# Kernel optimization log

Hardware: AMD Instinct MI355X
Metric: run time of the kernel (lower is better)

The kernel has to match this reference:

```python
import jax, jax.numpy as jnp
import numpy as np

ALPHA = 0.2  # LeakyReLU slope in GAT
OUT_SLOPE = 0.01  # default nn.LeakyyReLU slope for self.out
B, E, IN_DIM, HID, HEADS = 4, 2048, 32, 18, 3
DH = HID // HEADS  # per-head out dim = 6


def _leaky(x, slope):
    return jnp.where(x > 0, x, slope * x)


def _gat_head(x, adj, W, a):
    # x: [B,E,in], W: [in,dh], a: [2*dh,1]
    h = jnp.einsum('bei,id->bed', x, W)                      # [B,E,dh]
    d = h.shape[-1]
    # score[b,i,j] = leakyrelu(a . concat(h_i, h_j)) = leakyrelu(h_i.a1 + h_j.a2)
    e1 = jnp.einsum('bed,d->be', h, a[:d, 0])
    e2 = jnp.einsum('bed,d->be', h, a[d:, 0])
    score = _leaky(e1[:, :, None] + e2[:, None, :], ALPHA)   # [B,E,E]
    scores = jnp.where(adj == 1.0, score, 0.0)
    logits = jnp.where(adj > 0.0, scores, -30.0)
    att = jax.nn.softmax(logits, axis=2)                     # softmax over j
    # h_prime[b,j,d] = sum_i att[b,i,j] * h[b,i,d]  (torch sums over dim=1)
    h_prime = jnp.einsum('bij,bid->bjd', att, h)
    return jax.nn.elu(h_prime)  # concat=True -> elu


def _gat_multihead(x, adj, Ws, As):
    # Ws: [H,in,dh], As: [H,2*dh,1]
    outs = jax.vmap(lambda W, a: _gat_head(x, adj, W, a))(Ws, As)  # [H,B,E,dh]
    H, b, e, d = outs.shape
    return jnp.moveaxis(outs, 0, 2).reshape(b, e, H * d)  # concat heads last-dim


def _gcn(x, adj2d, W, b):
    return adj2d @ (x @ W) + b


def setup_inputs() -> dict:
    key = jax.random.key(0)
    ks = jax.random.split(key, 16)
    node_input = jax.random.normal(ks[0], (B, E, IN_DIM), jnp.float32)
    uv_filed = jax.random.normal(ks[1], (B, E, IN_DIM), jnp.float32)
    adj = jax.random.randint(ks[2], (B, E, E), 0, 2).astype(jnp.float32)
    s = 0.1
    Wt1 = jax.random.normal(ks[3], (HEADS, IN_DIM, DH), jnp.float32) * s
    at1 = jax.random.normal(ks[4], (HEADS, 2 * DH, 1), jnp.float32) * s
    Wt2 = jax.random.normal(ks[5], (HEADS, IN_DIM, DH), jnp.float32) * s
    at2 = jax.random.normal(ks[6], (HEADS, 2 * DH, 1), jnp.float32) * s
    Wg1 = jax.random.normal(ks[7], (HID, 16), jnp.float32) * s
    bg1 = jnp.zeros((16,), jnp.float32)
    Wg2 = jax.random.normal(ks[8], (16, 2), jnp.float32) * s
    bg2 = jnp.zeros((2,), jnp.float32)
    Wo1 = jax.random.normal(ks[9], (HID, 16), jnp.float32) * s
    bo1 = jnp.zeros((16,), jnp.float32)
    Wo2 = jax.random.normal(ks[10], (16, 2), jnp.float32) * s
    bo2 = jnp.zeros((2,), jnp.float32)
    return dict(node_input=node_input, uv_filed=uv_filed, adj=adj,
                Wt1=Wt1, at1=at1, Wt2=Wt2, at2=at2,
                Wg1=Wg1, bg1=bg1, Wg2=Wg2, bg2=bg2,
                Wo1=Wo1, bo1=bo1, Wo2=Wo2, bo2=bo2)


def reference(node_input, uv_filed, adj, Wt1, at1, Wt2, at2,
              Wg1, bg1, Wg2, bg2, Wo1, bo1, Wo2, bo2):
    h = _gat_multihead(node_input, adj, Wt1, at1)  # [B,E,18]
    o = _gat_multihead(uv_filed, adj, Wt2, at2)    # [B,E,18]
    a0 = adj[0]
    Y = jax.nn.relu(_gcn(h[0], a0, Wg1, bg1))
    O = jax.nn.relu(_gcn(o[0], a0, Wo1, bo1))
    Y = _gcn(Y, a0, Wg2, bg2)
    O = _gcn(O, a0, Wo2, bo2)
    return (jax.nn.log_softmax(Y, axis=1), _leaky(O, OUT_SLOPE))
```

## Files before the change

### kernel.cpp

```cpp
#include <hip/hip_runtime.h>
#include <hip/hip_bf16.h>


__global__ __launch_bounds__(256) void k0_bitmask(
    const float* __restrict__ adj0, unsigned int* __restrict__ bm) {
  int lane = threadIdx.x & 63, w = threadIdx.x >> 6;
  int row = blockIdx.x * 4 + w;
  const float* arow = adj0 + (size_t)row * 2048;
#pragma unroll 4
  for (int it = 0; it < 32; ++it) {
    float v = arow[it * 64 + lane];
    unsigned long long mask = __ballot(v == 1.0f);
    if (lane == 0) bm[row * 64 + it * 2] = (unsigned int)mask;
    else if (lane == 32) bm[row * 64 + it * 2 + 1] = (unsigned int)(mask >> 32);
  }
}

__global__ __launch_bounds__(256) void k1_features(
    const float* __restrict__ node, const float* __restrict__ uv,
    const float* __restrict__ Wt1, const float* __restrict__ at1,
    const float* __restrict__ Wt2, const float* __restrict__ at2,
    float* __restrict__ hcol, float* __restrict__ pack1, float* __restrict__ pack2) {
  __shared__ float sW[192];
  __shared__ float sA[12];
  int b = blockIdx.x;
  int g = b / 24;
  int h = (b / 8) % 3;
  int e = (b % 8) * 256 + threadIdx.x;
  const float* W = (g ? Wt2 : Wt1) + h * 192;
  const float* A = (g ? at2 : at1) + h * 12;
  const float* x = (g ? uv : node) + e * 32;
  if (threadIdx.x < 192) sW[threadIdx.x] = W[threadIdx.x];
  if (threadIdx.x < 12) sA[threadIdx.x] = A[threadIdx.x];
  __syncthreads();
  float xv[32];
#pragma unroll
  for (int i = 0; i < 32; ++i) xv[i] = x[i];
  float hv[6];
#pragma unroll
  for (int d = 0; d < 6; ++d) hv[d] = 0.f;
#pragma unroll
  for (int i = 0; i < 32; ++i)
#pragma unroll
    for (int d = 0; d < 6; ++d) hv[d] += xv[i] * sW[i * 6 + d];
  float e1 = 0.f, e2 = 0.f;
#pragma unroll
  for (int d = 0; d < 6; ++d) {
    e1 += hv[d] * sA[d];
    e2 += hv[d] * sA[6 + d];
  }
  int c = g * 3 + h;
#pragma unroll
  for (int d = 0; d < 6; ++d) hcol[(c * 6 + d) * 2048 + e] = hv[d];
  pack1[c * 2048 + e] = e1;
  pack1[(6 + c) * 2048 + e] = __expf(e1);
  pack1[(12 + c) * 2048 + e] = __expf(0.2f * e1);
  pack2[c * 2048 + e] = e2;
  pack2[(6 + c) * 2048 + e] = __expf(e2);
  pack2[(12 + c) * 2048 + e] = __expf(0.2f * e2);
}

__global__ __launch_bounds__(384) void k2_rowsum(
    const unsigned int* __restrict__ bm, const float* __restrict__ pack1,
    const float* __restrict__ pack2, float* __restrict__ invrs) {
  int tid = threadIdx.x;
  int c = tid >> 6, lane = tid & 63;
  int i0 = blockIdx.x * 8;
  const float4* p2_4 = (const float4*)pack2;
  float e1r[8], p1r[8], q1r[8], sum[8];
#pragma unroll
  for (int r = 0; r < 8; ++r) {
    e1r[r] = pack1[c * 2048 + i0 + r];
    p1r[r] = pack1[(6 + c) * 2048 + i0 + r];
    q1r[r] = pack1[(12 + c) * 2048 + i0 + r];
    sum[r] = 0.f;
  }
  int sh = (lane & 7) * 4;
#pragma unroll
  for (int it = 0; it < 8; ++it) {
    int j4 = it * 64 + lane;
    float4 e2 = p2_4[c * 512 + j4];
    float4 p2 = p2_4[(6 + c) * 512 + j4];
    float4 q2 = p2_4[(12 + c) * 512 + j4];
    int wbase = it * 8 + (lane >> 3);
    float abx, aby, abz, abw;
#pragma unroll
    for (int r = 0; r < 8; ++r) {
      unsigned int wd = bm[(i0 + r) * 64 + wbase] >> sh;
      { float e = e1r[r] + e2.x; bool p = e > 0.f;
        abx = (p ? p1r[r] : q1r[r]) * (p ? p2.x : q2.x); }
      { float e = e1r[r] + e2.y; bool p = e > 0.f;
        aby = (p ? p1r[r] : q1r[r]) * (p ? p2.y : q2.y); }
      { float e = e1r[r] + e2.z; bool p = e > 0.f;
        abz = (p ? p1r[r] : q1r[r]) * (p ? p2.z : q2.z); }
      { float e = e1r[r] + e2.w; bool p = e > 0.f;
        abw = (p ? p1r[r] : q1r[r]) * (p ? p2.w : q2.w); }
      float s = ((wd & 1u) ? abx : 0.f) + ((wd & 2u) ? aby : 0.f) +
                ((wd & 4u) ? abz : 0.f) + ((wd & 8u) ? abw : 0.f);
      sum[r] += s;
    }
  }
#pragma unroll
  for (int r = 0; r < 8; ++r) {
#pragma unroll
    for (int off = 32; off > 0; off >>= 1) sum[r] += __shfl_down(sum[r], off);
  }
  if (lane == 0) {
#pragma unroll
    for (int r = 0; r < 8; ++r) invrs[c * 2048 + i0 + r] = 1.0f / sum[r];
  }
}

__global__ __launch_bounds__(384) void k3_hprime(
    const unsigned int* __restrict__ bm, const float* __restrict__ hcol,
    const float* __restrict__ pack1, const float* __restrict__ pack2,
    const float* __restrict__ invrs, float* __restrict__ hp_part) {
  __shared__ float4 sPack[6 * 64];
  __shared__ float sHS[6 * 64 * 8];
  __shared__ unsigned int sM[64 * 4];
  float4* sHS4 = (float4*)sHS;
  int tid = threadIdx.x;
  int c6 = tid >> 6, jl = tid & 63;
  int j0 = blockIdx.x * 128;
  int jA = j0 + jl, jB = jA + 64;
  float e2A = pack2[c6 * 2048 + jA];
  float p2A = pack2[(6 + c6) * 2048 + jA];
  float q2A = pack2[(12 + c6) * 2048 + jA];
  float e2B = pack2[c6 * 2048 + jB];
  float p2B = pack2[(6 + c6) * 2048 + jB];
  float q2B = pack2[(12 + c6) * 2048 + jB];
  float aA0 = 0.f, aA1 = 0.f, aA2 = 0.f, aA3 = 0.f, aA4 = 0.f, aA5 = 0.f;
  float aB0 = 0.f, aB1 = 0.f, aB2 = 0.f, aB3 = 0.f, aB4 = 0.f, aB5 = 0.f;
  int hi = jl >> 5;
  int shj = jl & 31;
  int ibeg = blockIdx.y * 128;
  for (int i0 = ibeg; i0 < ibeg + 128; i0 += 64) {
    __syncthreads();
    {
      int cc = c6, ii = jl;
      float e1 = pack1[cc * 2048 + i0 + ii];
      float p1 = pack1[(6 + cc) * 2048 + i0 + ii];
      float q1 = pack1[(12 + cc) * 2048 + i0 + ii];
      sPack[cc * 64 + ii] = make_float4(e1, p1, q1, 0.f);
      float iv = invrs[cc * 2048 + i0 + ii];
#pragma unroll
      for (int d = 0; d < 6; ++d)
        sHS[(cc * 64 + ii) * 8 + d] = hcol[(cc * 6 + d) * 2048 + i0 + ii] * iv;
      sHS[(cc * 64 + ii) * 8 + 6] = 0.f;
      sHS[(cc * 64 + ii) * 8 + 7] = 0.f;
    }
    if (tid < 256) sM[tid] = bm[(size_t)(i0 + (tid >> 2)) * 64 + (j0 >> 5) + (tid & 3)];
    __syncthreads();
#pragma unroll 8
    for (int ii = 0; ii < 64; ++ii) {
      float4 pk = sPack[c6 * 64 + ii];
      float4 h0 = sHS4[(c6 * 64 + ii) * 2];
      float4 h1 = sHS4[(c6 * 64 + ii) * 2 + 1];
      unsigned int wdA = sM[ii * 4 + hi];
      unsigned int wdB = sM[ii * 4 + 2 + hi];
      {
        float e = pk.x + e2A; bool p = e > 0.f;
        float ab = (p ? pk.y : pk.z) * (p ? p2A : q2A);
        float wgt = ((wdA >> shj) & 1u) ? ab : 0.f;
        aA0 += wgt * h0.x; aA1 += wgt * h0.y; aA2 += wgt * h0.z;
        aA3 += wgt * h0.w; aA4 += wgt * h1.x; aA5 += wgt * h1.y;
      }
      {
        float e = pk.x + e2B; bool p = e > 0.f;
        float ab = (p ? pk.y : pk.z) * (p ? p2B : q2B);
        float wgt = ((wdB >> shj) & 1u) ? ab : 0.f;
        aB0 += wgt * h0.x; aB1 += wgt * h0.y; aB2 += wgt * h0.z;
        aB3 += wgt * h0.w; aB4 += wgt * h1.x; aB5 += wgt * h1.y;
      }
    }
  }
  float* hp = hp_part + (size_t)blockIdx.y * 73728;
  int kb = c6 * 6;
  hp[(kb + 0) * 2048 + jA] = aA0;
  hp[(kb + 1) * 2048 + jA] = aA1;
  hp[(kb + 2) * 2048 + jA] = aA2;
  hp[(kb + 3) * 2048 + jA] = aA3;
  hp[(kb + 4) * 2048 + jA] = aA4;
  hp[(kb + 5) * 2048 + jA] = aA5;
  hp[(kb + 0) * 2048 + jB] = aB0;
  hp[(kb + 1) * 2048 + jB] = aB1;
  hp[(kb + 2) * 2048 + jB] = aB2;
  hp[(kb + 3) * 2048 + jB] = aB3;
  hp[(kb + 4) * 2048 + jB] = aB4;
  hp[(kb + 5) * 2048 + jB] = aB5;
}

__global__ __launch_bounds__(256) void k4_T(
    const float* __restrict__ hp_part, const float* __restrict__ Wg1,
    const float* __restrict__ Wo1, float* __restrict__ T) {
  __shared__ float sHP[16 * 37];
  __shared__ float sWg[288], sWo[288];
  int tid = threadIdx.x;
  int j0 = blockIdx.x * 16;
  for (int idx = tid; idx < 288; idx += 256) {
    sWg[idx] = Wg1[idx];
    sWo[idx] = Wo1[idx];
  }
  for (int idx = tid; idx < 576; idx += 256) {
    int r = idx >> 4, jl = idx & 15;
    float s = 0.f;
#pragma unroll
    for (int sp = 0; sp < 16; ++sp)
      s += hp_part[(size_t)sp * 73728 + r * 2048 + j0 + jl];
    sHP[jl * 37 + r] = s;
  }
  __syncthreads();
  int jl = tid & 15, wq = tid >> 4;
  int gat = wq >> 3;
  int c0 = (wq & 7) * 2;
  const float* Wp = gat ? sWo : sWg;
  float a0 = 0.f, a1 = 0.f;
#pragma unroll
  for (int r = 0; r < 18; ++r) {
    float x = sHP[jl * 37 + gat * 18 + r];
    float hc = x > 0.f ? x : __expf(x) - 1.f;
    a0 += hc * Wp[r * 16 + c0];
    a1 += hc * Wp[r * 16 + c0 + 1];
  }
  T[(j0 + jl) * 32 + gat * 16 + c0] = a0;
  T[(j0 + jl) * 32 + gat * 16 + c0 + 1] = a1;
}

__global__ __launch_bounds__(256) void k5_gcn1(
    const unsigned int* __restrict__ bm, const float* __restrict__ T,
    float* __restrict__ Craw_part) {
  __shared__ unsigned int sM[64 * 4];
  __shared__ float4 sT4[128 * 8];
  const float4* T4 = (const float4*)T;
  int tid = threadIdx.x;
  int rl = tid & 31, cg = tid >> 5;
  int i0 = blockIdx.x * 64;
  int k0 = blockIdx.y * 128;
  if (tid < 256) sM[tid] = bm[(size_t)(i0 + (tid >> 2)) * 64 + (k0 >> 5) + (tid & 3)];
  for (int idx = tid; idx < 1024; idx += 256) sT4[idx] = T4[k0 * 8 + idx];
  __syncthreads();
  float a0x = 0.f, a0y = 0.f, a0z = 0.f, a0w = 0.f;
  float a1x = 0.f, a1y = 0.f, a1z = 0.f, a1w = 0.f;
#pragma unroll
  for (int wi = 0; wi < 4; ++wi) {
    unsigned int wA = sM[rl * 4 + wi];
    unsigned int wB = sM[(rl + 32) * 4 + wi];
#pragma unroll 16
    for (int kb = 0; kb < 32; ++kb) {
      float4 t = sT4[(wi * 32 + kb) * 8 + cg];
      float mA = (float)((wA >> kb) & 1u);
      float mB = (float)((wB >> kb) & 1u);
      a0x += mA * t.x; a0y += mA * t.y; a0z += mA * t.z; a0w += mA * t.w;
      a1x += mB * t.x; a1y += mB * t.y; a1z += mB * t.z; a1w += mB * t.w;
    }
  }
  float* base = Craw_part + (size_t)blockIdx.y * 65536;
  *(float4*)&base[(i0 + rl) * 32 + cg * 4] = make_float4(a0x, a0y, a0z, a0w);
  *(float4*)&base[(i0 + rl + 32) * 32 + cg * 4] = make_float4(a1x, a1y, a1z, a1w);
}

__global__ __launch_bounds__(256) void k6_T2(
    const float* __restrict__ Craw_part, const float* __restrict__ bg1,
    const float* __restrict__ Wg2, const float* __restrict__ bo1,
    const float* __restrict__ Wo2, float* __restrict__ T2) {
  int tid = threadIdx.x;
  int wave = tid >> 6, lane = tid & 63;
  int j = blockIdx.x * 8 + wave * 2 + (lane >> 5);
  int cl = lane & 31;
  int gat = cl >> 4, cc = cl & 15;
  float x = 0.f;
#pragma unroll
  for (int sp = 0; sp < 16; ++sp) x += Craw_part[(size_t)sp * 65536 + j * 32 + cl];
  x += gat ? bo1[cc] : bg1[cc];
  x = x > 0.f ? x : 0.f;
  float wa = gat ? Wo2[cc * 2 + 0] : Wg2[cc * 2 + 0];
  float wb = gat ? Wo2[cc * 2 + 1] : Wg2[cc * 2 + 1];
  float pa = x * wa, pb = x * wb;
#pragma unroll
  for (int m = 8; m > 0; m >>= 1) {
    pa += __shfl_xor(pa, m);
    pb += __shfl_xor(pb, m);
  }
  if (cc == 0) {
    T2[j * 4 + gat * 2 + 0] = pa;
    T2[j * 4 + gat * 2 + 1] = pb;
  }
}

__global__ __launch_bounds__(256) void k7_final(
    const unsigned int* __restrict__ bm, const float* __restrict__ T2,
    const float* __restrict__ bg2, const float* __restrict__ bo2,
    float* __restrict__ out) {
  int tid = threadIdx.x;
  int lane = tid & 63, w = tid >> 6;
  int r = blockIdx.x * 4 + w;
  const float4* T24 = (const float4*)T2;
  float4 acc = make_float4(0.f, 0.f, 0.f, 0.f);
  int sh = lane & 31;
#pragma unroll 8
  for (int it = 0; it < 32; ++it) {
    int k = it * 64 + lane;
    unsigned int wd = bm[r * 64 + it * 2 + (lane >> 5)];
    float m = (float)((wd >> sh) & 1u);
    float4 t = T24[k];
    acc.x += m * t.x;
    acc.y += m * t.y;
    acc.z += m * t.z;
    acc.w += m * t.w;
  }
#pragma unroll
  for (int off = 32; off > 0; off >>= 1) {
    acc.x += __shfl_down(acc.x, off);
    acc.y += __shfl_down(acc.y, off);
    acc.z += __shfl_down(acc.z, off);
    acc.w += __shfl_down(acc.w, off);
  }
  if (lane == 0) {
    float y0 = acc.x + bg2[0], y1 = acc.y + bg2[1];
    float m = fmaxf(y0, y1);
    float ls = m + logf(__expf(y0 - m) + __expf(y1 - m));
    out[r * 2 + 0] = y0 - ls;
    out[r * 2 + 1] = y1 - ls;
    float o0 = acc.z + bo2[0], o1 = acc.w + bo2[1];
    out[4096 + r * 2 + 0] = o0 > 0.f ? o0 : 0.01f * o0;
    out[4096 + r * 2 + 1] = o1 > 0.f ? o1 : 0.01f * o1;
  }
}

extern "C" void kernel_launch(void* const* d_in, const int* in_sizes, int n_in,
                              void* d_out, int out_size, void* d_ws, size_t ws_size,
                              hipStream_t stream) {
  const float* node = (const float*)d_in[0];
  const float* uv = (const float*)d_in[1];
  const float* adj = (const float*)d_in[2];
  const float* Wt1 = (const float*)d_in[3];
  const float* at1 = (const float*)d_in[4];
  const float* Wt2 = (const float*)d_in[5];
  const float* at2 = (const float*)d_in[6];
  const float* Wg1 = (const float*)d_in[7];
  const float* bg1 = (const float*)d_in[8];
  const float* Wg2 = (const float*)d_in[9];
  const float* bg2 = (const float*)d_in[10];
  const float* Wo1 = (const float*)d_in[11];
  const float* bo1 = (const float*)d_in[12];
  const float* Wo2 = (const float*)d_in[13];
  const float* bo2 = (const float*)d_in[14];
  float* ws = (float*)d_ws;
  float* hcol = ws;
  float* pack1 = ws + 73728;
  float* pack2 = ws + 110592;
  float* invrs = ws + 147456;
  float* T = ws + 159744;
  float* T2 = ws + 225280;
  unsigned int* bm = (unsigned int*)(ws + 233472);
  float* hp_part = ws + 364544;
  float* Craw_part = ws + 1544192;
  float* out = (float*)d_out;

  k0_bitmask<<<512, 256, 0, stream>>>(adj, bm);
  k1_features<<<48, 256, 0, stream>>>(node, uv, Wt1, at1, Wt2, at2, hcol, pack1, pack2);
  k2_rowsum<<<256, 384, 0, stream>>>(bm, pack1, pack2, invrs);
  k3_hprime<<<dim3(16, 16), 384, 0, stream>>>(bm, hcol, pack1, pack2, invrs, hp_part);
  k4_T<<<128, 256, 0, stream>>>(hp_part, Wg1, Wo1, T);
  k5_gcn1<<<dim3(32, 16), 256, 0, stream>>>(bm, T, Craw_part);
  k6_T2<<<256, 256, 0, stream>>>(Craw_part, bg1, Wg2, bo1, Wo2, T2);
  k7_final<<<512, 256, 0, stream>>>(bm, T2, bg2, bo2, out);
}
```

Before: 183.6 us.

## Fuse bitmask/feature and GCN1/T2 kernels, retile h-prime and rowsum grids

Merges the adjacency bitmask and feature kernels into one launch, and folds the GCN layer-1 split-K partial sums plus the T2 projection into a single kernel that loops over all K chunks, removing the Craw_part buffer. The h-prime kernel now handles 256 columns by 64 rows per block with no inner i loop, using 32 i-splits. The rowsum and T kernels get smaller per-block work for more blocks, and ELU is applied during the partial-sum reduction. The aim is fewer launches and less intermediate traffic, at the cost of lower parallelism in the fused GCN kernel (256 blocks, serial K) and more partials to reduce in k4.

```diff
diff --git a/kernel.cpp b/kernel.cpp
--- a/kernel.cpp
+++ b/kernel.cpp
@@ -2,31 +2,32 @@
 #include <hip/hip_bf16.h>
 
 
-__global__ __launch_bounds__(256) void k0_bitmask(
-    const float* __restrict__ adj0, unsigned int* __restrict__ bm) {
-  int lane = threadIdx.x & 63, w = threadIdx.x >> 6;
-  int row = blockIdx.x * 4 + w;
-  const float* arow = adj0 + (size_t)row * 2048;
-#pragma unroll 4
-  for (int it = 0; it < 32; ++it) {
-    float v = arow[it * 64 + lane];
-    unsigned long long mask = __ballot(v == 1.0f);
-    if (lane == 0) bm[row * 64 + it * 2] = (unsigned int)mask;
-    else if (lane == 32) bm[row * 64 + it * 2 + 1] = (unsigned int)(mask >> 32);
-  }
-}
-
-__global__ __launch_bounds__(256) void k1_features(
+__global__ __launch_bounds__(256) void k01(
+    const float* __restrict__ adj0, unsigned int* __restrict__ bm,
     const float* __restrict__ node, const float* __restrict__ uv,
     const float* __restrict__ Wt1, const float* __restrict__ at1,
     const float* __restrict__ Wt2, const float* __restrict__ at2,
     float* __restrict__ hcol, float* __restrict__ pack1, float* __restrict__ pack2) {
+  int b = blockIdx.x;
+  if (b < 512) {
+    int lane = threadIdx.x & 63, w = threadIdx.x >> 6;
+    int row = b * 4 + w;
+    const float* arow = adj0 + (size_t)row * 2048;
+#pragma unroll 4
+    for (int it = 0; it < 32; ++it) {
+      float v = arow[it * 64 + lane];
+      unsigned long long mask = __ballot(v == 1.0f);
+      if (lane == 0) bm[row * 64 + it * 2] = (unsigned int)mask;
+      else if (lane == 32) bm[row * 64 + it * 2 + 1] = (unsigned int)(mask >> 32);
+    }
+    return;
+  }
   __shared__ float sW[192];
   __shared__ float sA[12];
-  int b = blockIdx.x;
-  int g = b / 24;
-  int h = (b / 8) % 3;
-  int e = (b % 8) * 256 + threadIdx.x;
+  int fb = b - 512;
+  int g = fb / 24;
+  int h = (fb / 8) % 3;
+  int e = (fb % 8) * 256 + threadIdx.x;
   const float* W = (g ? Wt2 : Wt1) + h * 192;
   const float* A = (g ? at2 : at1) + h * 12;
   const float* x = (g ? uv : node) + e * 32;
@@ -65,11 +66,11 @@
     const float* __restrict__ pack2, float* __restrict__ invrs) {
   int tid = threadIdx.x;
   int c = tid >> 6, lane = tid & 63;
-  int i0 = blockIdx.x * 8;
+  int i0 = blockIdx.x * 4;
   const float4* p2_4 = (const float4*)pack2;
-  float e1r[8], p1r[8], q1r[8], sum[8];
-#pragma unroll
-  for (int r = 0; r < 8; ++r) {
+  float e1r[4], p1r[4], q1r[4], sum[4];
+#pragma unroll
+  for (int r = 0; r < 4; ++r) {
     e1r[r] = pack1[c * 2048 + i0 + r];
     p1r[r] = pack1[(6 + c) * 2048 + i0 + r];
     q1r[r] = pack1[(12 + c) * 2048 + i0 + r];
@@ -85,7 +86,7 @@
     int wbase = it * 8 + (lane >> 3);
     float abx, aby, abz, abw;
 #pragma unroll
-    for (int r = 0; r < 8; ++r) {
+    for (int r = 0; r < 4; ++r) {
       unsigned int wd = bm[(i0 + r) * 64 + wbase] >> sh;
       { float e = e1r[r] + e2.x; bool p = e > 0.f;
         abx = (p ? p1r[r] : q1r[r]) * (p ? p2.x : q2.x); }
@@ -101,13 +102,13 @@
     }
   }
 #pragma unroll
-  for (int r = 0; r < 8; ++r) {
+  for (int r = 0; r < 4; ++r) {
 #pragma unroll
     for (int off = 32; off > 0; off >>= 1) sum[r] += __shfl_down(sum[r], off);
   }
   if (lane == 0) {
 #pragma unroll
-    for (int r = 0; r < 8; ++r) invrs[c * 2048 + i0 + r] = 1.0f / sum[r];
+    for (int r = 0; r < 4; ++r) invrs[c * 2048 + i0 + r] = 1.0f / sum[r];
   }
 }
 
@@ -117,173 +118,141 @@
     const float* __restrict__ invrs, float* __restrict__ hp_part) {
   __shared__ float4 sPack[6 * 64];
   __shared__ float sHS[6 * 64 * 8];
-  __shared__ unsigned int sM[64 * 4];
+  __shared__ unsigned int sM[64 * 8];
   float4* sHS4 = (float4*)sHS;
   int tid = threadIdx.x;
   int c6 = tid >> 6, jl = tid & 63;
-  int j0 = blockIdx.x * 128;
-  int jA = j0 + jl, jB = jA + 64;
-  float e2A = pack2[c6 * 2048 + jA];
-  float p2A = pack2[(6 + c6) * 2048 + jA];
-  float q2A = pack2[(12 + c6) * 2048 + jA];
-  float e2B = pack2[c6 * 2048 + jB];
-  float p2B = pack2[(6 + c6) * 2048 + jB];
-  float q2B = pack2[(12 + c6) * 2048 + jB];
-  float aA0 = 0.f, aA1 = 0.f, aA2 = 0.f, aA3 = 0.f, aA4 = 0.f, aA5 = 0.f;
-  float aB0 = 0.f, aB1 = 0.f, aB2 = 0.f, aB3 = 0.f, aB4 = 0.f, aB5 = 0.f;
+  int j0 = blockIdx.x * 256;
+  int i0 = blockIdx.y * 64;
+  float e2v[4], p2v[4], q2v[4];
+#pragma unroll
+  for (int q = 0; q < 4; ++q) {
+    int j = j0 + q * 64 + jl;
+    e2v[q] = pack2[c6 * 2048 + j];
+    p2v[q] = pack2[(6 + c6) * 2048 + j];
+    q2v[q] = pack2[(12 + c6) * 2048 + j];
+  }
+  {
+    int cc = c6, ii = jl;
+    float e1 = pack1[cc * 2048 + i0 + ii];
+    float p1 = pack1[(6 + cc) * 2048 + i0 + ii];
+    float q1 = pack1[(12 + cc) * 2048 + i0 + ii];
+    sPack[cc * 64 + ii] = make_float4(e1, p1, q1, 0.f);
+    float iv = invrs[cc * 2048 + i0 + ii];
+#pragma unroll
+    for (int d = 0; d < 6; ++d)
+      sHS[(cc * 64 + ii) * 8 + d] = hcol[(cc * 6 + d) * 2048 + i0 + ii] * iv;
+    sHS[(cc * 64 + ii) * 8 + 6] = 0.f;
+    sHS[(cc * 64 + ii) * 8 + 7] = 0.f;
+  }
+  for (int idx = tid; idx < 512; idx += 384)
+    sM[idx] = bm[(size_t)(i0 + (idx >> 3)) * 64 + (j0 >> 5) + (idx & 7)];
+  __syncthreads();
+  float acc[4][6];
+#pragma unroll
+  for (int q = 0; q < 4; ++q)
+#pragma unroll
+    for (int d = 0; d < 6; ++d) acc[q][d] = 0.f;
   int hi = jl >> 5;
   int shj = jl & 31;
-  int ibeg = blockIdx.y * 128;
-  for (int i0 = ibeg; i0 < ibeg + 128; i0 += 64) {
-    __syncthreads();
-    {
-      int cc = c6, ii = jl;
-      float e1 = pack1[cc * 2048 + i0 + ii];
-      float p1 = pack1[(6 + cc) * 2048 + i0 + ii];
-      float q1 = pack1[(12 + cc) * 2048 + i0 + ii];
-      sPack[cc * 64 + ii] = make_float4(e1, p1, q1, 0.f);
-      float iv = invrs[cc * 2048 + i0 + ii];
-#pragma unroll
-      for (int d = 0; d < 6; ++d)
-        sHS[(cc * 64 + ii) * 8 + d] = hcol[(cc * 6 + d) * 2048 + i0 + ii] * iv;
-      sHS[(cc * 64 + ii) * 8 + 6] = 0.f;
-      sHS[(cc * 64 + ii) * 8 + 7] = 0.f;
-    }
-    if (tid < 256) sM[tid] = bm[(size_t)(i0 + (tid >> 2)) * 64 + (j0 >> 5) + (tid & 3)];
-    __syncthreads();
-#pragma unroll 8
-    for (int ii = 0; ii < 64; ++ii) {
-      float4 pk = sPack[c6 * 64 + ii];
-      float4 h0 = sHS4[(c6 * 64 + ii) * 2];
-      float4 h1 = sHS4[(c6 * 64 + ii) * 2 + 1];
-      unsigned int wdA = sM[ii * 4 + hi];
-      unsigned int wdB = sM[ii * 4 + 2 + hi];
-      {
-        float e = pk.x + e2A; bool p = e > 0.f;
-        float ab = (p ? pk.y : pk.z) * (p ? p2A : q2A);
-        float wgt = ((wdA >> shj) & 1u) ? ab : 0.f;
-        aA0 += wgt * h0.x; aA1 += wgt * h0.y; aA2 += wgt * h0.z;
-        aA3 += wgt * h0.w; aA4 += wgt * h1.x; aA5 += wgt * h1.y;
-      }
-      {
-        float e = pk.x + e2B; bool p = e > 0.f;
-        float ab = (p ? pk.y : pk.z) * (p ? p2B : q2B);
-        float wgt = ((wdB >> shj) & 1u) ? ab : 0.f;
-        aB0 += wgt * h0.x; aB1 += wgt * h0.y; aB2 += wgt * h0.z;
-        aB3 += wgt * h0.w; aB4 += wgt * h1.x; aB5 += wgt * h1.y;
-      }
+#pragma unroll 4
+  for (int ii = 0; ii < 64; ++ii) {
+    float4 pk = sPack[c6 * 64 + ii];
+    float4 h0 = sHS4[(c6 * 64 + ii) * 2];
+    float4 h1 = sHS4[(c6 * 64 + ii) * 2 + 1];
+#pragma unroll
+    for (int q = 0; q < 4; ++q) {
+      unsigned int wd = sM[ii * 8 + q * 2 + hi];
+      float e = pk.x + e2v[q];
+      bool p = e > 0.f;
+      float ab = (p ? pk.y : pk.z) * (p ? p2v[q] : q2v[q]);
+      float wgt = ((wd >> shj) & 1u) ? ab : 0.f;
+      acc[q][0] += wgt * h0.x; acc[q][1] += wgt * h0.y;
+      acc[q][2] += wgt * h0.z; acc[q][3] += wgt * h0.w;
+      acc[q][4] += wgt * h1.x; acc[q][5] += wgt * h1.y;
     }
   }
   float* hp = hp_part + (size_t)blockIdx.y * 73728;
   int kb = c6 * 6;
-  hp[(kb + 0) * 2048 + jA] = aA0;
-  hp[(kb + 1) * 2048 + jA] = aA1;
-  hp[(kb + 2) * 2048 + jA] = aA2;
-  hp[(kb + 3) * 2048 + jA] = aA3;
-  hp[(kb + 4) * 2048 + jA] = aA4;
-  hp[(kb + 5) * 2048 + jA] = aA5;
-  hp[(kb + 0) * 2048 + jB] = aB0;
-  hp[(kb + 1) * 2048 + jB] = aB1;
-  hp[(kb + 2) * 2048 + jB] = aB2;
-  hp[(kb + 3) * 2048 + jB] = aB3;
-  hp[(kb + 4) * 2048 + jB] = aB4;
-  hp[(kb + 5) * 2048 + jB] = aB5;
+#pragma unroll
+  for (int q = 0; q < 4; ++q) {
+    int j = j0 + q * 64 + jl;
+#pragma unroll
+    for (int d = 0; d < 6; ++d) hp[(kb + d) * 2048 + j] = acc[q][d];
+  }
 }
 
 __global__ __launch_bounds__(256) void k4_T(
     const float* __restrict__ hp_part, const float* __restrict__ Wg1,
     const float* __restrict__ Wo1, float* __restrict__ T) {
-  __shared__ float sHP[16 * 37];
+  __shared__ float sHP[8 * 37];
   __shared__ float sWg[288], sWo[288];
   int tid = threadIdx.x;
-  int j0 = blockIdx.x * 16;
+  int j0 = blockIdx.x * 8;
   for (int idx = tid; idx < 288; idx += 256) {
     sWg[idx] = Wg1[idx];
     sWo[idx] = Wo1[idx];
   }
-  for (int idx = tid; idx < 576; idx += 256) {
-    int r = idx >> 4, jl = idx & 15;
+  for (int idx = tid; idx < 288; idx += 256) {
+    int r = idx >> 3, jl = idx & 7;
     float s = 0.f;
 #pragma unroll
-    for (int sp = 0; sp < 16; ++sp)
+    for (int sp = 0; sp < 32; ++sp)
       s += hp_part[(size_t)sp * 73728 + r * 2048 + j0 + jl];
-    sHP[jl * 37 + r] = s;
+    sHP[jl * 37 + r] = s > 0.f ? s : __expf(s) - 1.f;
   }
   __syncthreads();
-  int jl = tid & 15, wq = tid >> 4;
-  int gat = wq >> 3;
-  int c0 = (wq & 7) * 2;
+  int jl = tid >> 5, col = tid & 31;
+  int gat = col >> 4, cc = col & 15;
   const float* Wp = gat ? sWo : sWg;
-  float a0 = 0.f, a1 = 0.f;
-#pragma unroll
-  for (int r = 0; r < 18; ++r) {
-    float x = sHP[jl * 37 + gat * 18 + r];
-    float hc = x > 0.f ? x : __expf(x) - 1.f;
-    a0 += hc * Wp[r * 16 + c0];
-    a1 += hc * Wp[r * 16 + c0 + 1];
-  }
-  T[(j0 + jl) * 32 + gat * 16 + c0] = a0;
-  T[(j0 + jl) * 32 + gat * 16 + c0 + 1] = a1;
+  float a = 0.f;
+#pragma unroll
+  for (int r = 0; r < 18; ++r)
+    a += sHP[jl * 37 + gat * 18 + r] * Wp[r * 16 + cc];
+  T[(j0 + jl) * 32 + col] = a;
 }
 
 __global__ __launch_bounds__(256) void k5_gcn1(
     const unsigned int* __restrict__ bm, const float* __restrict__ T,
-    float* __restrict__ Craw_part) {
-  __shared__ unsigned int sM[64 * 4];
-  __shared__ float4 sT4[128 * 8];
+    const float* __restrict__ bg1, const float* __restrict__ Wg2,
+    const float* __restrict__ bo1, const float* __restrict__ Wo2,
+    float* __restrict__ T2) {
+  __shared__ float sT[128 * 32];
+  float4* sT4 = (float4*)sT;
   const float4* T4 = (const float4*)T;
   int tid = threadIdx.x;
-  int rl = tid & 31, cg = tid >> 5;
-  int i0 = blockIdx.x * 64;
-  int k0 = blockIdx.y * 128;
-  if (tid < 256) sM[tid] = bm[(size_t)(i0 + (tid >> 2)) * 64 + (k0 >> 5) + (tid & 3)];
-  for (int idx = tid; idx < 1024; idx += 256) sT4[idx] = T4[k0 * 8 + idx];
-  __syncthreads();
-  float a0x = 0.f, a0y = 0.f, a0z = 0.f, a0w = 0.f;
-  float a1x = 0.f, a1y = 0.f, a1z = 0.f, a1w = 0.f;
-#pragma unroll
-  for (int wi = 0; wi < 4; ++wi) {
-    unsigned int wA = sM[rl * 4 + wi];
-    unsigned int wB = sM[(rl + 32) * 4 + wi];
-#pragma unroll 16
+  int row = tid >> 5, c = tid & 31;
+  int r = blockIdx.x * 8 + row;
+  float acc = 0.f;
+  for (int ch = 0; ch < 16; ++ch) {
+    __syncthreads();
+    for (int idx = tid; idx < 1024; idx += 256) sT4[idx] = T4[ch * 1024 + idx];
+    __syncthreads();
+    unsigned int w0 = bm[r * 64 + ch * 4 + 0];
+    unsigned int w1 = bm[r * 64 + ch * 4 + 1];
+    unsigned int w2 = bm[r * 64 + ch * 4 + 2];
+    unsigned int w3 = bm[r * 64 + ch * 4 + 3];
+#pragma unroll 8
     for (int kb = 0; kb < 32; ++kb) {
-      float4 t = sT4[(wi * 32 + kb) * 8 + cg];
-      float mA = (float)((wA >> kb) & 1u);
-      float mB = (float)((wB >> kb) & 1u);
-      a0x += mA * t.x; a0y += mA * t.y; a0z += mA * t.z; a0w += mA * t.w;
-      a1x += mB * t.x; a1y += mB * t.y; a1z += mB * t.z; a1w += mB * t.w;
+      acc += ((w0 >> kb) & 1u) ? sT[(kb) * 32 + c] : 0.f;
+      acc += ((w1 >> kb) & 1u) ? sT[(32 + kb) * 32 + c] : 0.f;
+      acc += ((w2 >> kb) & 1u) ? sT[(64 + kb) * 32 + c] : 0.f;
+      acc += ((w3 >> kb) & 1u) ? sT[(96 + kb) * 32 + c] : 0.f;
     }
   }
-  float* base = Craw_part + (size_t)blockIdx.y * 65536;
-  *(float4*)&base[(i0 + rl) * 32 + cg * 4] = make_float4(a0x, a0y, a0z, a0w);
-  *(float4*)&base[(i0 + rl + 32) * 32 + cg * 4] = make_float4(a1x, a1y, a1z, a1w);
-}
-
-__global__ __launch_bounds__(256) void k6_T2(
-    const float* __restrict__ Craw_part, const float* __restrict__ bg1,
-    const float* __restrict__ Wg2, const float* __restrict__ bo1,
-    const float* __restrict__ Wo2, float* __restrict__ T2) {
-  int tid = threadIdx.x;
-  int wave = tid >> 6, lane = tid & 63;
-  int j = blockIdx.x * 8 + wave * 2 + (lane >> 5);
-  int cl = lane & 31;
-  int gat = cl >> 4, cc = cl & 15;
-  float x = 0.f;
-#pragma unroll
-  for (int sp = 0; sp < 16; ++sp) x += Craw_part[(size_t)sp * 65536 + j * 32 + cl];
-  x += gat ? bo1[cc] : bg1[cc];
+  int gat = c >> 4, cc = c & 15;
+  float x = acc + (gat ? bo1[cc] : bg1[cc]);
   x = x > 0.f ? x : 0.f;
-  float wa = gat ? Wo2[cc * 2 + 0] : Wg2[cc * 2 + 0];
-  float wb = gat ? Wo2[cc * 2 + 1] : Wg2[cc * 2 + 1];
-  float pa = x * wa, pb = x * wb;
+  float pa = x * (gat ? Wo2[cc * 2 + 0] : Wg2[cc * 2 + 0]);
+  float pb = x * (gat ? Wo2[cc * 2 + 1] : Wg2[cc * 2 + 1]);
 #pragma unroll
   for (int m = 8; m > 0; m >>= 1) {
     pa += __shfl_xor(pa, m);
     pb += __shfl_xor(pb, m);
   }
   if (cc == 0) {
-    T2[j * 4 + gat * 2 + 0] = pa;
-    T2[j * 4 + gat * 2 + 1] = pb;
+    T2[r * 4 + gat * 2 + 0] = pa;
+    T2[r * 4 + gat * 2 + 1] = pb;
   }
 }
 
@@ -354,15 +323,13 @@
   float* T2 = ws + 225280;
   unsigned int* bm = (unsigned int*)(ws + 233472);
   float* hp_part = ws + 364544;
-  float* Craw_part = ws + 1544192;
   float* out = (float*)d_out;
 
-  k0_bitmask<<<512, 256, 0, stream>>>(adj, bm);
-  k1_features<<<48, 256, 0, stream>>>(node, uv, Wt1, at1, Wt2, at2, hcol, pack1, pack2);
-  k2_rowsum<<<256, 384, 0, stream>>>(bm, pack1, pack2, invrs);
-  k3_hprime<<<dim3(16, 16), 384, 0, stream>>>(bm, hcol, pack1, pack2, invrs, hp_part);
-  k4_T<<<128, 256, 0, stream>>>(hp_part, Wg1, Wo1, T);
-  k5_gcn1<<<dim3(32, 16), 256, 0, stream>>>(bm, T, Craw_part);
-  k6_T2<<<256, 256, 0, stream>>>(Craw_part, bg1, Wg2, bo1, Wo2, T2);
+  k01<<<560, 256, 0, stream>>>(adj, bm, node, uv, Wt1, at1, Wt2, at2,
+                               hcol, pack1, pack2);
+  k2_rowsum<<<512, 384, 0, stream>>>(bm, pack1, pack2, invrs);
+  k3_hprime<<<dim3(8, 32), 384, 0, stream>>>(bm, hcol, pack1, pack2, invrs, hp_part);
+  k4_T<<<256, 256, 0, stream>>>(hp_part, Wg1, Wo1, T);
+  k5_gcn1<<<256, 256, 0, stream>>>(bm, T, bg1, Wg2, bo1, Wo2, T2);
   k7_final<<<512, 256, 0, stream>>>(bm, T2, bg2, bo2, out);
 }
```

Result: slower. 233.1 us (+26.9%).
